# Kernel optimization log

Measured on AMD Instinct MI355X. Metric: run time of the kernel, lower is better.

## Reference

```python
import jax, jax.numpy as jnp
import numpy as np

N_NODES = 10000
N_EDGES = 640000
D_IN, D_HID, D_OUT = 128, 128, 64


def setup_inputs() -> dict:
    key = jax.random.key(0)
    ks = jax.random.split(key, 12)
    inp = {
        "inputs": jax.random.normal(ks[0], (N_NODES, D_IN), dtype=jnp.float32),
        "W_self0": jax.random.normal(ks[1], (D_IN, D_HID), dtype=jnp.float32) / np.sqrt(D_IN),
        "W_neigh0": jax.random.normal(ks[2], (D_IN, D_HID), dtype=jnp.float32) / np.sqrt(D_IN),
        "b0": jnp.zeros((D_HID,), dtype=jnp.float32),
        "W_self1": jax.random.normal(ks[3], (D_HID, D_HID), dtype=jnp.float32) / np.sqrt(D_HID),
        "W_neigh1": jax.random.normal(ks[4], (D_HID, D_HID), dtype=jnp.float32) / np.sqrt(D_HID),
        "b1": jnp.zeros((D_HID,), dtype=jnp.float32),
        "W_self2": jax.random.normal(ks[5], (D_HID, D_OUT), dtype=jnp.float32) / np.sqrt(D_HID),
        "W_neigh2": jax.random.normal(ks[6], (D_HID, D_OUT), dtype=jnp.float32) / np.sqrt(D_HID),
        "b2": jnp.zeros((D_OUT,), dtype=jnp.float32),
        "edge_src": jax.random.randint(ks[7], (N_EDGES,), 0, N_NODES, dtype=jnp.int32),
        "edge_dst": jax.random.randint(ks[8], (N_EDGES,), 0, N_NODES, dtype=jnp.int32),
    }
    return inp


def _sage_conv(h, W_self, W_neigh, b, edge_src, edge_dst):
    # mean aggregation: mean of source-node features over incoming edges at dst
    gathered = h[edge_src]                                   # [E, d] irregular gather
    agg = jax.ops.segment_sum(gathered, edge_dst, num_segments=N_NODES)  # [N, d]
    deg = jax.ops.segment_sum(jnp.ones((edge_dst.shape[0],), h.dtype), edge_dst,
                              num_segments=N_NODES)          # [N]
    h_neigh = agg / jnp.maximum(deg, 1.0)[:, None]
    return h @ W_self + h_neigh @ W_neigh + b


def reference(inputs, W_self0, W_neigh0, b0, W_self1, W_neigh1, b1,
              W_self2, W_neigh2, b2, edge_src, edge_dst):
    # dropout p=0.0 -> identity
    h = _sage_conv(inputs, W_self0, W_neigh0, b0, edge_src, edge_dst)
    h = jax.nn.relu(h)
    h = _sage_conv(h, W_self1, W_neigh1, b1, edge_src, edge_dst)
    h = jax.nn.relu(h)
    h = _sage_conv(h, W_self2, W_neigh2, b2, edge_src, edge_dst)
    return h
```

## Files before the change

kernel.cpp:

```cpp
#include <hip/hip_runtime.h>


#define NN 10000
#define NE 640000
#define NBINS 313
#define NBLKA 250
#define CHUNK 2560
#define SORT_CAP 4096

typedef __attribute__((ext_vector_type(8))) short s8v;
typedef __attribute__((ext_vector_type(4))) float f4v;

__device__ __forceinline__ ushort f2bf(float f) {
    unsigned u = __float_as_uint(f);
    return (ushort)((u + 0x7FFFu + ((u >> 16) & 1u)) >> 16);
}
__device__ __forceinline__ unsigned pack2(float a, float b) {
    return (unsigned)f2bf(a) | ((unsigned)f2bf(b) << 16);
}
__device__ __forceinline__ float bf_lo(unsigned u) { return __uint_as_float(u << 16); }
__device__ __forceinline__ float bf_hi(unsigned u) { return __uint_as_float(u & 0xFFFF0000u); }


__global__ void hist_prep_k(const int* __restrict__ edst, int* __restrict__ blockhist,
                            const float* __restrict__ x, ushort* __restrict__ xb,
                            const float* __restrict__ Ws0, const float* __restrict__ Wn0,
                            const float* __restrict__ Ws1, const float* __restrict__ Wn1,
                            const float* __restrict__ Ws2, const float* __restrict__ Wn2,
                            ushort* __restrict__ wt) {
    __shared__ int h[NBINS];
    int blk = blockIdx.x, tid = threadIdx.x;
    if (blk < NBLKA) {
        for (int i = tid; i < NBINS; i += 256) h[i] = 0;
        __syncthreads();
        int base = blk * CHUNK;
        for (int i = tid; i < CHUNK; i += 256)
            atomicAdd(&h[edst[base + i] >> 5], 1);
        __syncthreads();
        for (int i = tid; i < NBINS; i += 256)
            blockhist[blk * NBINS + i] = h[i];
    } else if (blk < NBLKA + 64) {
        int cb = blk - NBLKA;
        const float4* xv = (const float4*)x;
        uint2* xo = (uint2*)xb;
        for (int i = tid; i < 5000; i += 256) {
            int idx = cb * 5000 + i;
            float4 v = xv[idx];
            xo[idx] = make_uint2(pack2(v.x, v.y), pack2(v.z, v.w));
        }
    } else {
        int m = blk - NBLKA - 64;
        const float* W = (m == 0) ? Ws0 : (m == 1) ? Wn0 : (m == 2) ? Ws1
                       : (m == 3) ? Wn1 : (m == 4) ? Ws2 : Wn2;
        int MC = (m < 4) ? 128 : 64;
        ushort* dst = wt + ((m < 4) ? m * 16384 : 65536 + (m - 4) * 8192);
        int tot = 128 * MC;
        for (int idx = tid; idx < tot; idx += 256) {
            int k = (MC == 128) ? (idx >> 7) : (idx >> 6);
            int n = (MC == 128) ? (idx & 127) : (idx & 63);
            dst[n * 128 + k] = f2bf(W[idx]);
        }
    }
}


__global__ void scatter_k(const int* __restrict__ src, const int* __restrict__ dst,
                          const int* __restrict__ blockhist,
                          int* __restrict__ binstart_g, unsigned* __restrict__ tmp) {
    __shared__ int sa[512], sb[512];
    __shared__ int cur[NBINS];
    int blk = blockIdx.x, tid = threadIdx.x;
    int bin0 = tid, bin1 = tid + 256;
    int stot0 = 0, smine0 = 0, stot1 = 0, smine1 = 0;
    for (int b = 0; b < NBLKA; ++b) {
        int v0 = blockhist[b * NBINS + bin0];
        int v1 = (bin1 < NBINS) ? blockhist[b * NBINS + bin1] : 0;
        stot0 += v0; stot1 += v1;
        if (b < blk) { smine0 += v0; smine1 += v1; }
    }
    sa[bin0] = stot0; sa[bin1] = stot1;
    __syncthreads();
    int* pa = sa; int* pb = sb;
    for (int off = 1; off < 512; off <<= 1) {
        int x0 = pa[bin0] + ((bin0 >= off) ? pa[bin0 - off] : 0);
        int x1 = pa[bin1] + ((bin1 >= off) ? pa[bin1 - off] : 0);
        pb[bin0] = x0; pb[bin1] = x1;
        __syncthreads();
        int* t = pa; pa = pb; pb = t;
    }
    int bs0 = pa[bin0] - stot0;
    cur[bin0] = bs0 + smine0;
    int bs1 = 0;
    if (bin1 < NBINS) { bs1 = pa[bin1] - stot1; cur[bin1] = bs1 + smine1; }
    if (blk == 0) {
        binstart_g[bin0] = bs0;
        if (bin1 < NBINS) binstart_g[bin1] = bs1;
        if (tid == 0) binstart_g[NBINS] = pa[NBINS - 1];
    }
    __syncthreads();
    int base = blk * CHUNK;
    for (int i = tid; i < CHUNK; i += 256) {
        int d = dst[base + i], s = src[base + i];
        int pos = atomicAdd(&cur[d >> 5], 1);
        tmp[pos] = ((unsigned)s << 5) | (unsigned)(d & 31);
    }
}


__device__ void bin_sort_body(const unsigned* __restrict__ tmp,
                              const int* __restrict__ binstart,
                              int* __restrict__ offs, int* __restrict__ ssrc,
                              int b, int* stage) {
    __shared__ int cnt32[32];
    __shared__ int cur32[32];
    int tid = threadIdx.x;
    int beg = binstart[b], end = binstart[b + 1], cnt = end - beg;
    if (tid < 32) cnt32[tid] = 0;
    __syncthreads();
    for (int i = tid; i < cnt; i += 256)
        atomicAdd(&cnt32[tmp[beg + i] & 31], 1);
    __syncthreads();
    if (tid == 0) {
        int run = 0;
        for (int i = 0; i < 32; ++i) {
            int node = b * 32 + i;
            if (node < NN) offs[node] = beg + run;
            cur32[i] = run;
            run += cnt32[i];
        }
        if (b == NBINS - 1) offs[NN] = end;
    }
    __syncthreads();
    if (cnt <= SORT_CAP) {
        for (int i = tid; i < cnt; i += 256) {
            unsigned p = tmp[beg + i];
            int pos = atomicAdd(&cur32[p & 31], 1);
            stage[pos] = (int)(p >> 5);
        }
        __syncthreads();
        for (int i = tid; i < cnt; i += 256)
            ssrc[beg + i] = stage[i];
    } else {
        for (int i = tid; i < cnt; i += 256) {
            unsigned p = tmp[beg + i];
            int pos = atomicAdd(&cur32[p & 31], 1);
            ssrc[beg + pos] = (int)(p >> 5);
        }
    }
}

__global__ void sort_dense0_k(const unsigned* __restrict__ tmp, const int* __restrict__ binstart,
                              int* __restrict__ offs, int* __restrict__ ssrc,
                              const ushort* __restrict__ xb, const ushort* __restrict__ wt,
                              const float* __restrict__ b0,
                              float* __restrict__ hs, ushort* __restrict__ hn) {
    __shared__ int stage[SORT_CAP];
    int blk = blockIdx.x;
    if (blk < NBINS) { bin_sort_body(tmp, binstart, offs, ssrc, blk, stage); return; }

    int dblk = blk - NBINS;
    int l = threadIdx.x & 63, w = threadIdx.x >> 6;
    int mloc = l & 15, quad = l >> 4;
    int row_base = dblk * 32 + (w & 1) * 16;
    int colh = w >> 1;
    int arow = row_base + mloc;
    int arow_c = (arow < NN) ? arow : (NN - 1);
    const ushort* wsT = wt;
    const ushort* wnT = wt + 16384;
    f4v accS[4], accN[4];
#pragma unroll
    for (int nt = 0; nt < 4; ++nt) { accS[nt] = (f4v){0,0,0,0}; accN[nt] = (f4v){0,0,0,0}; }
#pragma unroll
    for (int ks = 0; ks < 4; ++ks) {
        int kb = ks * 32 + quad * 8;
        s8v a = *(const s8v*)(xb + (size_t)arow_c * 128 + kb);
#pragma unroll
        for (int nt = 0; nt < 4; ++nt) {
            int n = colh * 64 + nt * 16 + mloc;
            s8v bs = *(const s8v*)(wsT + n * 128 + kb);
            s8v bn = *(const s8v*)(wnT + n * 128 + kb);
            accS[nt] = __builtin_amdgcn_mfma_f32_16x16x32_bf16(a, bs, accS[nt], 0, 0, 0);
            accN[nt] = __builtin_amdgcn_mfma_f32_16x16x32_bf16(a, bn, accN[nt], 0, 0, 0);
        }
    }
#pragma unroll
    for (int nt = 0; nt < 4; ++nt) {
        int col = colh * 64 + nt * 16 + mloc;
        float bv = b0[col];
#pragma unroll
        for (int r = 0; r < 4; ++r) {
            int row = row_base + quad * 4 + r;
            if (row < NN) {
                hs[(size_t)row * 128 + col] = accS[nt][r] + bv;
                hn[(size_t)row * 128 + col] = f2bf(accN[nt][r]);
            }
        }
    }
}


template <int MOUT>
__global__ void agg_dense_k(const float* __restrict__ hs_in, const ushort* __restrict__ hn_in,
                            const int* __restrict__ offs, const int* __restrict__ ssrc,
                            const ushort* __restrict__ wsT, const ushort* __restrict__ wnT,
                            const float* __restrict__ bias,
                            float* __restrict__ hs_out, ushort* __restrict__ hn_out) {
    __shared__ ushort hrow[16 * 136];
    int tid = threadIdx.x;
    int node_loc = tid >> 4, t = tid & 15;
    int node = blockIdx.x * 16 + node_loc;
    int beg = offs[node], end = offs[node + 1];
    const uint4* hn4 = (const uint4*)hn_in;
    float a0 = 0, a1 = 0, a2 = 0, a3 = 0, a4 = 0, a5 = 0, a6 = 0, a7 = 0;
    int e = beg;
    for (; e + 4 <= end; e += 4) {
        int s0 = ssrc[e], s1 = ssrc[e + 1], s2 = ssrc[e + 2], s3 = ssrc[e + 3];
        uint4 v0 = hn4[(size_t)s0 * 16 + t];
        uint4 v1 = hn4[(size_t)s1 * 16 + t];
        uint4 v2 = hn4[(size_t)s2 * 16 + t];
        uint4 v3 = hn4[(size_t)s3 * 16 + t];
        a0 += bf_lo(v0.x) + bf_lo(v1.x) + bf_lo(v2.x) + bf_lo(v3.x);
        a1 += bf_hi(v0.x) + bf_hi(v1.x) + bf_hi(v2.x) + bf_hi(v3.x);
        a2 += bf_lo(v0.y) + bf_lo(v1.y) + bf_lo(v2.y) + bf_lo(v3.y);
        a3 += bf_hi(v0.y) + bf_hi(v1.y) + bf_hi(v2.y) + bf_hi(v3.y);
        a4 += bf_lo(v0.z) + bf_lo(v1.z) + bf_lo(v2.z) + bf_lo(v3.z);
        a5 += bf_hi(v0.z) + bf_hi(v1.z) + bf_hi(v2.z) + bf_hi(v3.z);
        a6 += bf_lo(v0.w) + bf_lo(v1.w) + bf_lo(v2.w) + bf_lo(v3.w);
        a7 += bf_hi(v0.w) + bf_hi(v1.w) + bf_hi(v2.w) + bf_hi(v3.w);
    }
    for (; e < end; ++e) {
        uint4 v = hn4[(size_t)ssrc[e] * 16 + t];
        a0 += bf_lo(v.x); a1 += bf_hi(v.x); a2 += bf_lo(v.y); a3 += bf_hi(v.y);
        a4 += bf_lo(v.z); a5 += bf_hi(v.z); a6 += bf_lo(v.w); a7 += bf_hi(v.w);
    }
    int deg = end - beg;
    float sc = 1.0f / (float)(deg > 0 ? deg : 1);
    float4 h4a = ((const float4*)hs_in)[(size_t)node * 32 + 2 * t];
    float4 h4b = ((const float4*)hs_in)[(size_t)node * 32 + 2 * t + 1];
    float r0 = fmaxf(h4a.x + a0 * sc, 0.f), r1 = fmaxf(h4a.y + a1 * sc, 0.f);
    float r2 = fmaxf(h4a.z + a2 * sc, 0.f), r3 = fmaxf(h4a.w + a3 * sc, 0.f);
    float r4 = fmaxf(h4b.x + a4 * sc, 0.f), r5 = fmaxf(h4b.y + a5 * sc, 0.f);
    float r6 = fmaxf(h4b.z + a6 * sc, 0.f), r7 = fmaxf(h4b.w + a7 * sc, 0.f);
    *(uint4*)(hrow + node_loc * 136 + t * 8) =
        make_uint4(pack2(r0, r1), pack2(r2, r3), pack2(r4, r5), pack2(r6, r7));
    __syncthreads();

    int l = tid & 63, w = tid >> 6;
    int mloc = l & 15, quad = l >> 4;
    constexpr int NTPW = MOUT / 64;
    f4v accS[NTPW], accN[NTPW];
#pragma unroll
    for (int nt = 0; nt < NTPW; ++nt) { accS[nt] = (f4v){0,0,0,0}; accN[nt] = (f4v){0,0,0,0}; }
#pragma unroll
    for (int ks = 0; ks < 4; ++ks) {
        int kb = ks * 32 + quad * 8;
        s8v a = *(const s8v*)(hrow + mloc * 136 + kb);
#pragma unroll
        for (int nt = 0; nt < NTPW; ++nt) {
            int n = (w * NTPW + nt) * 16 + mloc;
            s8v bs = *(const s8v*)(wsT + n * 128 + kb);
            s8v bn = *(const s8v*)(wnT + n * 128 + kb);
            accS[nt] = __builtin_amdgcn_mfma_f32_16x16x32_bf16(a, bs, accS[nt], 0, 0, 0);
            accN[nt] = __builtin_amdgcn_mfma_f32_16x16x32_bf16(a, bn, accN[nt], 0, 0, 0);
        }
    }
#pragma unroll
    for (int nt = 0; nt < NTPW; ++nt) {
        int col = (w * NTPW + nt) * 16 + mloc;
        float bv = bias[col];
#pragma unroll
        for (int r = 0; r < 4; ++r) {
            int row = blockIdx.x * 16 + quad * 4 + r;
            hs_out[(size_t)row * MOUT + col] = accS[nt][r] + bv;
            hn_out[(size_t)row * MOUT + col] = f2bf(accN[nt][r]);
        }
    }
}


__global__ void agg_out_k(const float* __restrict__ hs_in, const ushort* __restrict__ hn_in,
                          const int* __restrict__ offs, const int* __restrict__ ssrc,
                          float* __restrict__ out) {
    int tid = threadIdx.x;
    int node = blockIdx.x * 32 + (tid >> 3);
    int t = tid & 7;
    if (node >= NN) return;
    int beg = offs[node], end = offs[node + 1];
    const uint4* hn4 = (const uint4*)hn_in;
    float a0 = 0, a1 = 0, a2 = 0, a3 = 0, a4 = 0, a5 = 0, a6 = 0, a7 = 0;
    int e = beg;
    for (; e + 4 <= end; e += 4) {
        int s0 = ssrc[e], s1 = ssrc[e + 1], s2 = ssrc[e + 2], s3 = ssrc[e + 3];
        uint4 v0 = hn4[(size_t)s0 * 8 + t];
        uint4 v1 = hn4[(size_t)s1 * 8 + t];
        uint4 v2 = hn4[(size_t)s2 * 8 + t];
        uint4 v3 = hn4[(size_t)s3 * 8 + t];
        a0 += bf_lo(v0.x) + bf_lo(v1.x) + bf_lo(v2.x) + bf_lo(v3.x);
        a1 += bf_hi(v0.x) + bf_hi(v1.x) + bf_hi(v2.x) + bf_hi(v3.x);
        a2 += bf_lo(v0.y) + bf_lo(v1.y) + bf_lo(v2.y) + bf_lo(v3.y);
        a3 += bf_hi(v0.y) + bf_hi(v1.y) + bf_hi(v2.y) + bf_hi(v3.y);
        a4 += bf_lo(v0.z) + bf_lo(v1.z) + bf_lo(v2.z) + bf_lo(v3.z);
        a5 += bf_hi(v0.z) + bf_hi(v1.z) + bf_hi(v2.z) + bf_hi(v3.z);
        a6 += bf_lo(v0.w) + bf_lo(v1.w) + bf_lo(v2.w) + bf_lo(v3.w);
        a7 += bf_hi(v0.w) + bf_hi(v1.w) + bf_hi(v2.w) + bf_hi(v3.w);
    }
    for (; e < end; ++e) {
        uint4 v = hn4[(size_t)ssrc[e] * 8 + t];
        a0 += bf_lo(v.x); a1 += bf_hi(v.x); a2 += bf_lo(v.y); a3 += bf_hi(v.y);
        a4 += bf_lo(v.z); a5 += bf_hi(v.z); a6 += bf_lo(v.w); a7 += bf_hi(v.w);
    }
    int deg = end - beg;
    float sc = 1.0f / (float)(deg > 0 ? deg : 1);
    float4 h4a = ((const float4*)hs_in)[(size_t)node * 16 + 2 * t];
    float4 h4b = ((const float4*)hs_in)[(size_t)node * 16 + 2 * t + 1];
    ((float4*)out)[(size_t)node * 16 + 2 * t] =
        make_float4(h4a.x + a0 * sc, h4a.y + a1 * sc, h4a.z + a2 * sc, h4a.w + a3 * sc);
    ((float4*)out)[(size_t)node * 16 + 2 * t + 1] =
        make_float4(h4b.x + a4 * sc, h4b.y + a5 * sc, h4b.z + a6 * sc, h4b.w + a7 * sc);
}


extern "C" void kernel_launch(void* const* d_in, const int* in_sizes, int n_in,
                              void* d_out, int out_size, void* d_ws, size_t ws_size,
                              hipStream_t stream) {
    const float* x   = (const float*)d_in[0];
    const float* Ws0 = (const float*)d_in[1];
    const float* Wn0 = (const float*)d_in[2];
    const float* b0  = (const float*)d_in[3];
    const float* Ws1 = (const float*)d_in[4];
    const float* Wn1 = (const float*)d_in[5];
    const float* b1  = (const float*)d_in[6];
    const float* Ws2 = (const float*)d_in[7];
    const float* Wn2 = (const float*)d_in[8];
    const float* b2  = (const float*)d_in[9];
    const int* esrc  = (const int*)d_in[10];
    const int* edst  = (const int*)d_in[11];
    float* out = (float*)d_out;

    float*  hsA = (float*)d_ws;
    float*  hsB = hsA + (size_t)NN * 128;
    ushort* hnA = (ushort*)(hsB + (size_t)NN * 128);
    ushort* hnB = hnA + (size_t)NN * 128;
    ushort* xb  = hnB + (size_t)NN * 128;
    ushort* wt  = xb + (size_t)NN * 128;
    unsigned* tmp = (unsigned*)(wt + 81920);
    int* ssrc = (int*)(tmp + NE);
    int* offs = ssrc + NE;
    int* blockhist = offs + NN + 1;
    int* binstart = blockhist + NBLKA * NBINS;

    const ushort* wt0s = wt;
    const ushort* wt0n = wt + 16384;
    const ushort* wt1s = wt + 32768;
    const ushort* wt1n = wt + 49152;
    const ushort* wt2s = wt + 65536;
    const ushort* wt2n = wt + 73728;

    hist_prep_k<<<NBLKA + 64 + 6, 256, 0, stream>>>(edst, blockhist, x, xb,
                                                    Ws0, Wn0, Ws1, Wn1, Ws2, Wn2, wt);
    scatter_k<<<NBLKA, 256, 0, stream>>>(esrc, edst, blockhist, binstart, tmp);
    sort_dense0_k<<<NBINS + 313, 256, 0, stream>>>(tmp, binstart, offs, ssrc,
                                                   xb, wt, b0, hsA, hnA);
    agg_dense_k<128><<<NN / 16, 256, 0, stream>>>(hsA, hnA, offs, ssrc,
                                                  wt1s, wt1n, b1, hsB, hnB);
    agg_dense_k<64><<<NN / 16, 256, 0, stream>>>(hsB, hnB, offs, ssrc,
                                                 wt2s, wt2n, b2, hsA, hnA);
    agg_out_k<<<(NN + 31) / 32, 256, 0, stream>>>(hsA, hnA, offs, ssrc, out);
}
```

Measured before the change: 196.3 us.

## Merge all stages into one cooperative persistent kernel with grid syncs

The six separate kernel launches become a single cooperative kernel. Each former kernel is now a device-function phase run over a grid-stride loop, and the phases are separated by grid.sync(). The aim is to remove launch overhead and the gaps between kernels in a pipeline that is dominated by small stages. In exchange, parallelism is capped at the occupancy-limited grid size, five grid-wide barriers are added, and register and shared-memory pressure is shared across all phases under launch_bounds(256,2).

```diff
diff --git a/kernel.cpp b/kernel.cpp
--- a/kernel.cpp
+++ b/kernel.cpp
@@ -1,4 +1,7 @@
 #include <hip/hip_runtime.h>
+#include <hip/hip_cooperative_groups.h>
+
+namespace cg = cooperative_groups;
 
 
 #define NN 10000
@@ -21,60 +24,64 @@
 __device__ __forceinline__ float bf_lo(unsigned u) { return __uint_as_float(u << 16); }
 __device__ __forceinline__ float bf_hi(unsigned u) { return __uint_as_float(u & 0xFFFF0000u); }
 
-
-__global__ void hist_prep_k(const int* __restrict__ edst, int* __restrict__ blockhist,
-                            const float* __restrict__ x, ushort* __restrict__ xb,
-                            const float* __restrict__ Ws0, const float* __restrict__ Wn0,
-                            const float* __restrict__ Ws1, const float* __restrict__ Wn1,
-                            const float* __restrict__ Ws2, const float* __restrict__ Wn2,
-                            ushort* __restrict__ wt) {
-    __shared__ int h[NBINS];
-    int blk = blockIdx.x, tid = threadIdx.x;
-    if (blk < NBLKA) {
-        for (int i = tid; i < NBINS; i += 256) h[i] = 0;
-        __syncthreads();
-        int base = blk * CHUNK;
-        for (int i = tid; i < CHUNK; i += 256)
-            atomicAdd(&h[edst[base + i] >> 5], 1);
-        __syncthreads();
-        for (int i = tid; i < NBINS; i += 256)
-            blockhist[blk * NBINS + i] = h[i];
-    } else if (blk < NBLKA + 64) {
-        int cb = blk - NBLKA;
-        const float4* xv = (const float4*)x;
-        uint2* xo = (uint2*)xb;
-        for (int i = tid; i < 5000; i += 256) {
-            int idx = cb * 5000 + i;
-            float4 v = xv[idx];
-            xo[idx] = make_uint2(pack2(v.x, v.y), pack2(v.z, v.w));
-        }
-    } else {
-        int m = blk - NBLKA - 64;
-        const float* W = (m == 0) ? Ws0 : (m == 1) ? Wn0 : (m == 2) ? Ws1
-                       : (m == 3) ? Wn1 : (m == 4) ? Ws2 : Wn2;
-        int MC = (m < 4) ? 128 : 64;
-        ushort* dst = wt + ((m < 4) ? m * 16384 : 65536 + (m - 4) * 8192);
-        int tot = 128 * MC;
-        for (int idx = tid; idx < tot; idx += 256) {
-            int k = (MC == 128) ? (idx >> 7) : (idx >> 6);
-            int n = (MC == 128) ? (idx & 127) : (idx & 63);
-            dst[n * 128 + k] = f2bf(W[idx]);
-        }
-    }
-}
-
-
-__global__ void scatter_k(const int* __restrict__ src, const int* __restrict__ dst,
-                          const int* __restrict__ blockhist,
-                          int* __restrict__ binstart_g, unsigned* __restrict__ tmp) {
-    __shared__ int sa[512], sb[512];
-    __shared__ int cur[NBINS];
-    int blk = blockIdx.x, tid = threadIdx.x;
+struct Prm {
+    const int *esrc, *edst;
+    const float *x, *Ws0, *Wn0, *b0, *Ws1, *Wn1, *b1, *Ws2, *Wn2, *b2;
+    float* out;
+    float *hsA, *hsB;
+    ushort *hnA, *hnB, *xb, *wt;
+    unsigned* tmp;
+    int *ssrc, *offs, *blockhist, *binstart;
+};
+
+
+__device__ void hist_body(const Prm& p, int blk, int* smem) {
+    int* h = smem;
+    int tid = threadIdx.x;
+    for (int i = tid; i < NBINS; i += 256) h[i] = 0;
+    __syncthreads();
+    int base = blk * CHUNK;
+    for (int i = tid; i < CHUNK; i += 256)
+        atomicAdd(&h[p.edst[base + i] >> 5], 1);
+    __syncthreads();
+    for (int i = tid; i < NBINS; i += 256)
+        p.blockhist[blk * NBINS + i] = h[i];
+}
+
+__device__ void xconv_body(const Prm& p, int cb) {
+    const float4* xv = (const float4*)p.x;
+    uint2* xo = (uint2*)p.xb;
+    for (int i = threadIdx.x; i < 5000; i += 256) {
+        int idx = cb * 5000 + i;
+        float4 v = xv[idx];
+        xo[idx] = make_uint2(pack2(v.x, v.y), pack2(v.z, v.w));
+    }
+}
+
+__device__ void wconv_body(const Prm& p, int m) {
+    const float* W = (m == 0) ? p.Ws0 : (m == 1) ? p.Wn0 : (m == 2) ? p.Ws1
+                   : (m == 3) ? p.Wn1 : (m == 4) ? p.Ws2 : p.Wn2;
+    int MC = (m < 4) ? 128 : 64;
+    ushort* dst = p.wt + ((m < 4) ? m * 16384 : 65536 + (m - 4) * 8192);
+    int tot = 128 * MC;
+    for (int idx = threadIdx.x; idx < tot; idx += 256) {
+        int k = (MC == 128) ? (idx >> 7) : (idx >> 6);
+        int n = (MC == 128) ? (idx & 127) : (idx & 63);
+        dst[n * 128 + k] = f2bf(W[idx]);
+    }
+}
+
+
+__device__ void scatter_body(const Prm& p, int blk, int* smem) {
+    int* sa = smem;
+    int* sb = smem + 512;
+    int* cur = smem + 1024;
+    int tid = threadIdx.x;
     int bin0 = tid, bin1 = tid + 256;
     int stot0 = 0, smine0 = 0, stot1 = 0, smine1 = 0;
     for (int b = 0; b < NBLKA; ++b) {
-        int v0 = blockhist[b * NBINS + bin0];
-        int v1 = (bin1 < NBINS) ? blockhist[b * NBINS + bin1] : 0;
+        int v0 = p.blockhist[b * NBINS + bin0];
+        int v1 = (bin1 < NBINS) ? p.blockhist[b * NBINS + bin1] : 0;
         stot0 += v0; stot1 += v1;
         if (b < blk) { smine0 += v0; smine1 += v1; }
     }
@@ -93,87 +100,76 @@
     int bs1 = 0;
     if (bin1 < NBINS) { bs1 = pa[bin1] - stot1; cur[bin1] = bs1 + smine1; }
     if (blk == 0) {
-        binstart_g[bin0] = bs0;
-        if (bin1 < NBINS) binstart_g[bin1] = bs1;
-        if (tid == 0) binstart_g[NBINS] = pa[NBINS - 1];
+        p.binstart[bin0] = bs0;
+        if (bin1 < NBINS) p.binstart[bin1] = bs1;
+        if (tid == 0) p.binstart[NBINS] = pa[NBINS - 1];
     }
     __syncthreads();
     int base = blk * CHUNK;
     for (int i = tid; i < CHUNK; i += 256) {
-        int d = dst[base + i], s = src[base + i];
+        int d = p.edst[base + i], s = p.esrc[base + i];
         int pos = atomicAdd(&cur[d >> 5], 1);
-        tmp[pos] = ((unsigned)s << 5) | (unsigned)(d & 31);
-    }
-}
-
-
-__device__ void bin_sort_body(const unsigned* __restrict__ tmp,
-                              const int* __restrict__ binstart,
-                              int* __restrict__ offs, int* __restrict__ ssrc,
-                              int b, int* stage) {
-    __shared__ int cnt32[32];
-    __shared__ int cur32[32];
+        p.tmp[pos] = ((unsigned)s << 5) | (unsigned)(d & 31);
+    }
+}
+
+
+__device__ void sort_body(const Prm& p, int b, int* smem) {
+    int* stage = smem;
+    int* cnt32 = smem + SORT_CAP;
+    int* cur32 = smem + SORT_CAP + 32;
     int tid = threadIdx.x;
-    int beg = binstart[b], end = binstart[b + 1], cnt = end - beg;
+    int beg = p.binstart[b], end = p.binstart[b + 1], cnt = end - beg;
     if (tid < 32) cnt32[tid] = 0;
     __syncthreads();
     for (int i = tid; i < cnt; i += 256)
-        atomicAdd(&cnt32[tmp[beg + i] & 31], 1);
+        atomicAdd(&cnt32[p.tmp[beg + i] & 31], 1);
     __syncthreads();
     if (tid == 0) {
         int run = 0;
         for (int i = 0; i < 32; ++i) {
             int node = b * 32 + i;
-            if (node < NN) offs[node] = beg + run;
+            if (node < NN) p.offs[node] = beg + run;
             cur32[i] = run;
             run += cnt32[i];
         }
-        if (b == NBINS - 1) offs[NN] = end;
+        if (b == NBINS - 1) p.offs[NN] = end;
     }
     __syncthreads();
     if (cnt <= SORT_CAP) {
         for (int i = tid; i < cnt; i += 256) {
-            unsigned p = tmp[beg + i];
-            int pos = atomicAdd(&cur32[p & 31], 1);
-            stage[pos] = (int)(p >> 5);
+            unsigned q = p.tmp[beg + i];
+            int pos = atomicAdd(&cur32[q & 31], 1);
+            stage[pos] = (int)(q >> 5);
         }
         __syncthreads();
         for (int i = tid; i < cnt; i += 256)
-            ssrc[beg + i] = stage[i];
+            p.ssrc[beg + i] = stage[i];
     } else {
         for (int i = tid; i < cnt; i += 256) {
-            unsigned p = tmp[beg + i];
-            int pos = atomicAdd(&cur32[p & 31], 1);
-            ssrc[beg + pos] = (int)(p >> 5);
-        }
-    }
-}
-
-__global__ void sort_dense0_k(const unsigned* __restrict__ tmp, const int* __restrict__ binstart,
-                              int* __restrict__ offs, int* __restrict__ ssrc,
-                              const ushort* __restrict__ xb, const ushort* __restrict__ wt,
-                              const float* __restrict__ b0,
-                              float* __restrict__ hs, ushort* __restrict__ hn) {
-    __shared__ int stage[SORT_CAP];
-    int blk = blockIdx.x;
-    if (blk < NBINS) { bin_sort_body(tmp, binstart, offs, ssrc, blk, stage); return; }
-
-    int dblk = blk - NBINS;
+            unsigned q = p.tmp[beg + i];
+            int pos = atomicAdd(&cur32[q & 31], 1);
+            p.ssrc[beg + pos] = (int)(q >> 5);
+        }
+    }
+}
+
+__device__ void dense0_body(const Prm& p, int dblk) {
     int l = threadIdx.x & 63, w = threadIdx.x >> 6;
     int mloc = l & 15, quad = l >> 4;
     int row_base = dblk * 32 + (w & 1) * 16;
     int colh = w >> 1;
     int arow = row_base + mloc;
     int arow_c = (arow < NN) ? arow : (NN - 1);
-    const ushort* wsT = wt;
-    const ushort* wnT = wt + 16384;
+    const ushort* wsT = p.wt;
+    const ushort* wnT = p.wt + 16384;
     f4v accS[4], accN[4];
 #pragma unroll
     for (int nt = 0; nt < 4; ++nt) { accS[nt] = (f4v){0,0,0,0}; accN[nt] = (f4v){0,0,0,0}; }
 #pragma unroll
     for (int ks = 0; ks < 4; ++ks) {
         int kb = ks * 32 + quad * 8;
-        s8v a = *(const s8v*)(xb + (size_t)arow_c * 128 + kb);
+        s8v a = *(const s8v*)(p.xb + (size_t)arow_c * 128 + kb);
 #pragma unroll
         for (int nt = 0; nt < 4; ++nt) {
             int n = colh * 64 + nt * 16 + mloc;
@@ -186,13 +182,13 @@
 #pragma unroll
     for (int nt = 0; nt < 4; ++nt) {
         int col = colh * 64 + nt * 16 + mloc;
-        float bv = b0[col];
+        float bv = p.b0[col];
 #pragma unroll
         for (int r = 0; r < 4; ++r) {
             int row = row_base + quad * 4 + r;
             if (row < NN) {
-                hs[(size_t)row * 128 + col] = accS[nt][r] + bv;
-                hn[(size_t)row * 128 + col] = f2bf(accN[nt][r]);
+                p.hsA[(size_t)row * 128 + col] = accS[nt][r] + bv;
+                p.hnA[(size_t)row * 128 + col] = f2bf(accN[nt][r]);
             }
         }
     }
@@ -200,21 +196,21 @@
 
 
 template <int MOUT>
-__global__ void agg_dense_k(const float* __restrict__ hs_in, const ushort* __restrict__ hn_in,
-                            const int* __restrict__ offs, const int* __restrict__ ssrc,
-                            const ushort* __restrict__ wsT, const ushort* __restrict__ wnT,
-                            const float* __restrict__ bias,
-                            float* __restrict__ hs_out, ushort* __restrict__ hn_out) {
-    __shared__ ushort hrow[16 * 136];
+__device__ void agg_dense_body(const float* __restrict__ hs_in, const ushort* __restrict__ hn_in,
+                               const ushort* __restrict__ wsT, const ushort* __restrict__ wnT,
+                               const float* __restrict__ bias,
+                               float* __restrict__ hs_out, ushort* __restrict__ hn_out,
+                               const Prm& p, int item, int* smem) {
+    ushort* hrow = (ushort*)smem;
     int tid = threadIdx.x;
     int node_loc = tid >> 4, t = tid & 15;
-    int node = blockIdx.x * 16 + node_loc;
-    int beg = offs[node], end = offs[node + 1];
+    int node = item * 16 + node_loc;
+    int beg = p.offs[node], end = p.offs[node + 1];
     const uint4* hn4 = (const uint4*)hn_in;
     float a0 = 0, a1 = 0, a2 = 0, a3 = 0, a4 = 0, a5 = 0, a6 = 0, a7 = 0;
     int e = beg;
     for (; e + 4 <= end; e += 4) {
-        int s0 = ssrc[e], s1 = ssrc[e + 1], s2 = ssrc[e + 2], s3 = ssrc[e + 3];
+        int s0 = p.ssrc[e], s1 = p.ssrc[e + 1], s2 = p.ssrc[e + 2], s3 = p.ssrc[e + 3];
         uint4 v0 = hn4[(size_t)s0 * 16 + t];
         uint4 v1 = hn4[(size_t)s1 * 16 + t];
         uint4 v2 = hn4[(size_t)s2 * 16 + t];
@@ -229,7 +225,7 @@
         a7 += bf_hi(v0.w) + bf_hi(v1.w) + bf_hi(v2.w) + bf_hi(v3.w);
     }
     for (; e < end; ++e) {
-        uint4 v = hn4[(size_t)ssrc[e] * 16 + t];
+        uint4 v = hn4[(size_t)p.ssrc[e] * 16 + t];
         a0 += bf_lo(v.x); a1 += bf_hi(v.x); a2 += bf_lo(v.y); a3 += bf_hi(v.y);
         a4 += bf_lo(v.z); a5 += bf_hi(v.z); a6 += bf_lo(v.w); a7 += bf_hi(v.w);
     }
@@ -270,7 +266,7 @@
         float bv = bias[col];
 #pragma unroll
         for (int r = 0; r < 4; ++r) {
-            int row = blockIdx.x * 16 + quad * 4 + r;
+            int row = item * 16 + quad * 4 + r;
             hs_out[(size_t)row * MOUT + col] = accS[nt][r] + bv;
             hn_out[(size_t)row * MOUT + col] = f2bf(accN[nt][r]);
         }
@@ -278,19 +274,17 @@
 }
 
 
-__global__ void agg_out_k(const float* __restrict__ hs_in, const ushort* __restrict__ hn_in,
-                          const int* __restrict__ offs, const int* __restrict__ ssrc,
-                          float* __restrict__ out) {
+__device__ void agg_out_body(const Prm& p, int item) {
     int tid = threadIdx.x;
-    int node = blockIdx.x * 32 + (tid >> 3);
+    int node = item * 32 + (tid >> 3);
     int t = tid & 7;
     if (node >= NN) return;
-    int beg = offs[node], end = offs[node + 1];
-    const uint4* hn4 = (const uint4*)hn_in;
+    int beg = p.offs[node], end = p.offs[node + 1];
+    const uint4* hn4 = (const uint4*)p.hnA;
     float a0 = 0, a1 = 0, a2 = 0, a3 = 0, a4 = 0, a5 = 0, a6 = 0, a7 = 0;
     int e = beg;
     for (; e + 4 <= end; e += 4) {
-        int s0 = ssrc[e], s1 = ssrc[e + 1], s2 = ssrc[e + 2], s3 = ssrc[e + 3];
+        int s0 = p.ssrc[e], s1 = p.ssrc[e + 1], s2 = p.ssrc[e + 2], s3 = p.ssrc[e + 3];
         uint4 v0 = hn4[(size_t)s0 * 8 + t];
         uint4 v1 = hn4[(size_t)s1 * 8 + t];
         uint4 v2 = hn4[(size_t)s2 * 8 + t];
@@ -305,65 +299,103 @@
         a7 += bf_hi(v0.w) + bf_hi(v1.w) + bf_hi(v2.w) + bf_hi(v3.w);
     }
     for (; e < end; ++e) {
-        uint4 v = hn4[(size_t)ssrc[e] * 8 + t];
+        uint4 v = hn4[(size_t)p.ssrc[e] * 8 + t];
         a0 += bf_lo(v.x); a1 += bf_hi(v.x); a2 += bf_lo(v.y); a3 += bf_hi(v.y);
         a4 += bf_lo(v.z); a5 += bf_hi(v.z); a6 += bf_lo(v.w); a7 += bf_hi(v.w);
     }
     int deg = end - beg;
     float sc = 1.0f / (float)(deg > 0 ? deg : 1);
-    float4 h4a = ((const float4*)hs_in)[(size_t)node * 16 + 2 * t];
-    float4 h4b = ((const float4*)hs_in)[(size_t)node * 16 + 2 * t + 1];
-    ((float4*)out)[(size_t)node * 16 + 2 * t] =
+    float4 h4a = ((const float4*)p.hsA)[(size_t)node * 16 + 2 * t];
+    float4 h4b = ((const float4*)p.hsA)[(size_t)node * 16 + 2 * t + 1];
+    ((float4*)p.out)[(size_t)node * 16 + 2 * t] =
         make_float4(h4a.x + a0 * sc, h4a.y + a1 * sc, h4a.z + a2 * sc, h4a.w + a3 * sc);
-    ((float4*)out)[(size_t)node * 16 + 2 * t + 1] =
+    ((float4*)p.out)[(size_t)node * 16 + 2 * t + 1] =
         make_float4(h4b.x + a4 * sc, h4b.y + a5 * sc, h4b.z + a6 * sc, h4b.w + a7 * sc);
+}
+
+
+__global__ __launch_bounds__(256, 2) void mega_k(Prm p) {
+    __shared__ int smem[SORT_CAP + 64];
+    cg::grid_group grid = cg::this_grid();
+
+    for (int it = blockIdx.x; it < NBLKA + 64 + 6; it += gridDim.x) {
+        if (it < NBLKA) hist_body(p, it, smem);
+        else if (it < NBLKA + 64) xconv_body(p, it - NBLKA);
+        else wconv_body(p, it - NBLKA - 64);
+        __syncthreads();
+    }
+    grid.sync();
+
+    for (int it = blockIdx.x; it < NBLKA; it += gridDim.x) {
+        scatter_body(p, it, smem);
+        __syncthreads();
+    }
+    grid.sync();
+
+    for (int it = blockIdx.x; it < NBINS + 313; it += gridDim.x) {
+        if (it < NBINS) sort_body(p, it, smem);
+        else dense0_body(p, it - NBINS);
+        __syncthreads();
+    }
+    grid.sync();
+
+    for (int it = blockIdx.x; it < NN / 16; it += gridDim.x) {
+        agg_dense_body<128>(p.hsA, p.hnA, p.wt + 32768, p.wt + 49152, p.b1,
+                            p.hsB, p.hnB, p, it, smem);
+        __syncthreads();
+    }
+    grid.sync();
+
+    for (int it = blockIdx.x; it < NN / 16; it += gridDim.x) {
+        agg_dense_body<64>(p.hsB, p.hnB, p.wt + 65536, p.wt + 73728, p.b2,
+                           p.hsA, p.hnA, p, it, smem);
+        __syncthreads();
+    }
+    grid.sync();
+
+    for (int it = blockIdx.x; it < (NN + 31) / 32; it += gridDim.x)
+        agg_out_body(p, it);
 }
 
 
 extern "C" void kernel_launch(void* const* d_in, const int* in_sizes, int n_in,
                               void* d_out, int out_size, void* d_ws, size_t ws_size,
                               hipStream_t stream) {
-    const float* x   = (const float*)d_in[0];
-    const float* Ws0 = (const float*)d_in[1];
-    const float* Wn0 = (const float*)d_in[2];
-    const float* b0  = (const float*)d_in[3];
-    const float* Ws1 = (const float*)d_in[4];
-    const float* Wn1 = (const float*)d_in[5];
-    const float* b1  = (const float*)d_in[6];
-    const float* Ws2 = (const float*)d_in[7];
-    const float* Wn2 = (const float*)d_in[8];
-    const float* b2  = (const float*)d_in[9];
-    const int* esrc  = (const int*)d_in[10];
-    const int* edst  = (const int*)d_in[11];
-    float* out = (float*)d_out;
-
-    float*  hsA = (float*)d_ws;
-    float*  hsB = hsA + (size_t)NN * 128;
-    ushort* hnA = (ushort*)(hsB + (size_t)NN * 128);
-    ushort* hnB = hnA + (size_t)NN * 128;
-    ushort* xb  = hnB + (size_t)NN * 128;
-    ushort* wt  = xb + (size_t)NN * 128;
-    unsigned* tmp = (unsigned*)(wt + 81920);
-    int* ssrc = (int*)(tmp + NE);
-    int* offs = ssrc + NE;
-    int* blockhist = offs + NN + 1;
-    int* binstart = blockhist + NBLKA * NBINS;
-
-    const ushort* wt0s = wt;
-    const ushort* wt0n = wt + 16384;
-    const ushort* wt1s = wt + 32768;
-    const ushort* wt1n = wt + 49152;
-    const ushort* wt2s = wt + 65536;
-    const ushort* wt2n = wt + 73728;
-
-    hist_prep_k<<<NBLKA + 64 + 6, 256, 0, stream>>>(edst, blockhist, x, xb,
-                                                    Ws0, Wn0, Ws1, Wn1, Ws2, Wn2, wt);
-    scatter_k<<<NBLKA, 256, 0, stream>>>(esrc, edst, blockhist, binstart, tmp);
-    sort_dense0_k<<<NBINS + 313, 256, 0, stream>>>(tmp, binstart, offs, ssrc,
-                                                   xb, wt, b0, hsA, hnA);
-    agg_dense_k<128><<<NN / 16, 256, 0, stream>>>(hsA, hnA, offs, ssrc,
-                                                  wt1s, wt1n, b1, hsB, hnB);
-    agg_dense_k<64><<<NN / 16, 256, 0, stream>>>(hsB, hnB, offs, ssrc,
-                                                 wt2s, wt2n, b2, hsA, hnA);
-    agg_out_k<<<(NN + 31) / 32, 256, 0, stream>>>(hsA, hnA, offs, ssrc, out);
-}
+    Prm p;
+    p.x   = (const float*)d_in[0];
+    p.Ws0 = (const float*)d_in[1];
+    p.Wn0 = (const float*)d_in[2];
+    p.b0  = (const float*)d_in[3];
+    p.Ws1 = (const float*)d_in[4];
+    p.Wn1 = (const float*)d_in[5];
+    p.b1  = (const float*)d_in[6];
+    p.Ws2 = (const float*)d_in[7];
+    p.Wn2 = (const float*)d_in[8];
+    p.b2  = (const float*)d_in[9];
+    p.esrc = (const int*)d_in[10];
+    p.edst = (const int*)d_in[11];
+    p.out = (float*)d_out;
+
+    p.hsA = (float*)d_ws;
+    p.hsB = p.hsA + (size_t)NN * 128;
+    p.hnA = (ushort*)(p.hsB + (size_t)NN * 128);
+    p.hnB = p.hnA + (size_t)NN * 128;
+    p.xb  = p.hnB + (size_t)NN * 128;
+    p.wt  = p.xb + (size_t)NN * 128;
+    p.tmp = (unsigned*)(p.wt + 81920);
+    p.ssrc = (int*)(p.tmp + NE);
+    p.offs = p.ssrc + NE;
+    p.blockhist = p.offs + NN + 1;
+    p.binstart = p.blockhist + NBLKA * NBINS;
+
+    int bpc = 0;
+    hipError_t e = hipOccupancyMaxActiveBlocksPerMultiprocessor(
+        &bpc, reinterpret_cast<const void*>(mega_k), 256, 0);
+    if (e != hipSuccess || bpc < 1) bpc = 1;
+    int grid = bpc * 256;
+    if (grid > NBINS + 313) grid = NBINS + 313;
+
+    void* args[] = { &p };
+    hipLaunchCooperativeKernel(reinterpret_cast<const void*>(mega_k),
+                               dim3(grid), dim3(256), args, 0, stream);
+}
```

Measured after the change: 536.5 us. 173% more time.

## Co-schedule layer-0 dense GEMM with edge scatter and stage weight transpose in LDS

Applied to the files above, without the earlier changes.

The layer-0 dense MFMA blocks move out of the sort kernel and into the scatter kernel, so the dense work overlaps the edge scatter while the bin sort becomes its own kernel. The weight transpose now builds each transposed matrix in a 32KB shared buffer and writes it out coalesced, replacing strided global stores. The larger shared allocation in the prep kernel can lower occupancy for the histogram and convert blocks. The number of launches stays the same.

```diff
diff --git a/kernel.cpp b/kernel.cpp
--- a/kernel.cpp
+++ b/kernel.cpp
@@ -22,15 +22,16 @@
 __device__ __forceinline__ float bf_hi(unsigned u) { return __uint_as_float(u & 0xFFFF0000u); }
 
 
-__global__ void hist_prep_k(const int* __restrict__ edst, int* __restrict__ blockhist,
-                            const float* __restrict__ x, ushort* __restrict__ xb,
-                            const float* __restrict__ Ws0, const float* __restrict__ Wn0,
-                            const float* __restrict__ Ws1, const float* __restrict__ Wn1,
-                            const float* __restrict__ Ws2, const float* __restrict__ Wn2,
-                            ushort* __restrict__ wt) {
-    __shared__ int h[NBINS];
+__global__ void prep_k(const int* __restrict__ edst, int* __restrict__ blockhist,
+                       const float* __restrict__ x, ushort* __restrict__ xb,
+                       const float* __restrict__ Ws0, const float* __restrict__ Wn0,
+                       const float* __restrict__ Ws1, const float* __restrict__ Wn1,
+                       const float* __restrict__ Ws2, const float* __restrict__ Wn2,
+                       ushort* __restrict__ wt) {
+    __shared__ ushort ps[128 * 128];
     int blk = blockIdx.x, tid = threadIdx.x;
     if (blk < NBLKA) {
+        int* h = (int*)ps;
         for (int i = tid; i < NBINS; i += 256) h[i] = 0;
         __syncthreads();
         int base = blk * CHUNK;
@@ -58,18 +59,23 @@
         for (int idx = tid; idx < tot; idx += 256) {
             int k = (MC == 128) ? (idx >> 7) : (idx >> 6);
             int n = (MC == 128) ? (idx & 127) : (idx & 63);
-            dst[n * 128 + k] = f2bf(W[idx]);
-        }
-    }
-}
-
-
-__global__ void scatter_k(const int* __restrict__ src, const int* __restrict__ dst,
-                          const int* __restrict__ blockhist,
-                          int* __restrict__ binstart_g, unsigned* __restrict__ tmp) {
-    __shared__ int sa[512], sb[512];
-    __shared__ int cur[NBINS];
-    int blk = blockIdx.x, tid = threadIdx.x;
+            ps[n * 128 + k] = f2bf(W[idx]);
+        }
+        __syncthreads();
+        for (int idx = tid; idx < tot; idx += 256)
+            dst[idx] = ps[idx];
+    }
+}
+
+
+__device__ void scatter_body(const int* __restrict__ src, const int* __restrict__ dst,
+                             const int* __restrict__ blockhist,
+                             int* __restrict__ binstart_g, unsigned* __restrict__ tmp,
+                             int blk, int* smem) {
+    int* sa = smem;
+    int* sb = smem + 512;
+    int* cur = smem + 1024;
+    int tid = threadIdx.x;
     int bin0 = tid, bin1 = tid + 256;
     int stot0 = 0, smine0 = 0, stot1 = 0, smine1 = 0;
     for (int b = 0; b < NBLKA; ++b) {
@@ -106,59 +112,9 @@
     }
 }
 
-
-__device__ void bin_sort_body(const unsigned* __restrict__ tmp,
-                              const int* __restrict__ binstart,
-                              int* __restrict__ offs, int* __restrict__ ssrc,
-                              int b, int* stage) {
-    __shared__ int cnt32[32];
-    __shared__ int cur32[32];
-    int tid = threadIdx.x;
-    int beg = binstart[b], end = binstart[b + 1], cnt = end - beg;
-    if (tid < 32) cnt32[tid] = 0;
-    __syncthreads();
-    for (int i = tid; i < cnt; i += 256)
-        atomicAdd(&cnt32[tmp[beg + i] & 31], 1);
-    __syncthreads();
-    if (tid == 0) {
-        int run = 0;
-        for (int i = 0; i < 32; ++i) {
-            int node = b * 32 + i;
-            if (node < NN) offs[node] = beg + run;
-            cur32[i] = run;
-            run += cnt32[i];
-        }
-        if (b == NBINS - 1) offs[NN] = end;
-    }
-    __syncthreads();
-    if (cnt <= SORT_CAP) {
-        for (int i = tid; i < cnt; i += 256) {
-            unsigned p = tmp[beg + i];
-            int pos = atomicAdd(&cur32[p & 31], 1);
-            stage[pos] = (int)(p >> 5);
-        }
-        __syncthreads();
-        for (int i = tid; i < cnt; i += 256)
-            ssrc[beg + i] = stage[i];
-    } else {
-        for (int i = tid; i < cnt; i += 256) {
-            unsigned p = tmp[beg + i];
-            int pos = atomicAdd(&cur32[p & 31], 1);
-            ssrc[beg + pos] = (int)(p >> 5);
-        }
-    }
-}
-
-__global__ void sort_dense0_k(const unsigned* __restrict__ tmp, const int* __restrict__ binstart,
-                              int* __restrict__ offs, int* __restrict__ ssrc,
-                              const ushort* __restrict__ xb, const ushort* __restrict__ wt,
-                              const float* __restrict__ b0,
-                              float* __restrict__ hs, ushort* __restrict__ hn) {
-    __shared__ int stage[SORT_CAP];
-    int blk = blockIdx.x;
-    if (blk < NBINS) { bin_sort_body(tmp, binstart, offs, ssrc, blk, stage); return; }
-
-    int dblk = blk - NBINS;
+__device__ void dense0_body(const ushort* __restrict__ xb, const ushort* __restrict__ wt,
+                            const float* __restrict__ b0,
+                            float* __restrict__ hs, ushort* __restrict__ hn, int dblk) {
     int l = threadIdx.x & 63, w = threadIdx.x >> 6;
     int mloc = l & 15, quad = l >> 4;
     int row_base = dblk * 32 + (w & 1) * 16;
@@ -194,6 +150,62 @@
                 hs[(size_t)row * 128 + col] = accS[nt][r] + bv;
                 hn[(size_t)row * 128 + col] = f2bf(accN[nt][r]);
             }
+        }
+    }
+}
+
+__global__ void scatdense_k(const int* __restrict__ esrc, const int* __restrict__ edst,
+                            const int* __restrict__ blockhist, int* __restrict__ binstart,
+                            unsigned* __restrict__ tmp,
+                            const ushort* __restrict__ xb, const ushort* __restrict__ wt,
+                            const float* __restrict__ b0,
+                            float* __restrict__ hs, ushort* __restrict__ hn) {
+    __shared__ int smem[1024 + NBINS];
+    int blk = blockIdx.x;
+    if (blk < NBLKA)
+        scatter_body(esrc, edst, blockhist, binstart, tmp, blk, smem);
+    else
+        dense0_body(xb, wt, b0, hs, hn, blk - NBLKA);
+}
+
+
+__global__ void sort_k(const unsigned* __restrict__ tmp, const int* __restrict__ binstart,
+                       int* __restrict__ offs, int* __restrict__ ssrc) {
+    __shared__ int stage[SORT_CAP];
+    __shared__ int cnt32[32];
+    __shared__ int cur32[32];
+    int b = blockIdx.x, tid = threadIdx.x;
+    int beg = binstart[b], end = binstart[b + 1], cnt = end - beg;
+    if (tid < 32) cnt32[tid] = 0;
+    __syncthreads();
+    for (int i = tid; i < cnt; i += 256)
+        atomicAdd(&cnt32[tmp[beg + i] & 31], 1);
+    __syncthreads();
+    if (tid == 0) {
+        int run = 0;
+        for (int i = 0; i < 32; ++i) {
+            int node = b * 32 + i;
+            if (node < NN) offs[node] = beg + run;
+            cur32[i] = run;
+            run += cnt32[i];
+        }
+        if (b == NBINS - 1) offs[NN] = end;
+    }
+    __syncthreads();
+    if (cnt <= SORT_CAP) {
+        for (int i = tid; i < cnt; i += 256) {
+            unsigned q = tmp[beg + i];
+            int pos = atomicAdd(&cur32[q & 31], 1);
+            stage[pos] = (int)(q >> 5);
+        }
+        __syncthreads();
+        for (int i = tid; i < cnt; i += 256)
+            ssrc[beg + i] = stage[i];
+    } else {
+        for (int i = tid; i < cnt; i += 256) {
+            unsigned q = tmp[beg + i];
+            int pos = atomicAdd(&cur32[q & 31], 1);
+            ssrc[beg + pos] = (int)(q >> 5);
         }
     }
 }
@@ -349,21 +361,14 @@
     int* blockhist = offs + NN + 1;
     int* binstart = blockhist + NBLKA * NBINS;
 
-    const ushort* wt0s = wt;
-    const ushort* wt0n = wt + 16384;
-    const ushort* wt1s = wt + 32768;
-    const ushort* wt1n = wt + 49152;
-    const ushort* wt2s = wt + 65536;
-    const ushort* wt2n = wt + 73728;
-
-    hist_prep_k<<<NBLKA + 64 + 6, 256, 0, stream>>>(edst, blockhist, x, xb,
-                                                    Ws0, Wn0, Ws1, Wn1, Ws2, Wn2, wt);
-    scatter_k<<<NBLKA, 256, 0, stream>>>(esrc, edst, blockhist, binstart, tmp);
-    sort_dense0_k<<<NBINS + 313, 256, 0, stream>>>(tmp, binstart, offs, ssrc,
-                                                   xb, wt, b0, hsA, hnA);
+    prep_k<<<NBLKA + 64 + 6, 256, 0, stream>>>(edst, blockhist, x, xb,
+                                               Ws0, Wn0, Ws1, Wn1, Ws2, Wn2, wt);
+    scatdense_k<<<NBLKA + 313, 256, 0, stream>>>(esrc, edst, blockhist, binstart,
+                                                 tmp, xb, wt, b0, hsA, hnA);
+    sort_k<<<NBINS, 256, 0, stream>>>(tmp, binstart, offs, ssrc);
     agg_dense_k<128><<<NN / 16, 256, 0, stream>>>(hsA, hnA, offs, ssrc,
-                                                  wt1s, wt1n, b1, hsB, hnB);
+                                                  wt + 32768, wt + 49152, b1, hsB, hnB);
     agg_dense_k<64><<<NN / 16, 256, 0, stream>>>(hsB, hnB, offs, ssrc,
-                                                 wt2s, wt2n, b2, hsA, hnA);
+                                                 wt + 65536, wt + 73728, b2, hsA, hnA);
     agg_out_k<<<(NN + 31) / 32, 256, 0, stream>>>(hsA, hnA, offs, ssrc, out);
 }
```

After: 185.5 us. 1.06x faster.
